# Performance work log

Measured on AMD Instinct MI355X. Metric: run time of the kernel, lower is better.

## Reference

```python
import jax, jax.numpy as jnp
import numpy as np

TOP_K = 8


def setup_inputs() -> dict:
    key = jax.random.key(0)
    k1, k2, k3 = jax.random.split(key, 3)
    tokens, hidden, experts = 32768, 2048, 64
    hidden_states = jax.random.normal(k1, (tokens, hidden), dtype=jnp.float32)
    weight = jax.random.normal(k2, (experts, hidden), dtype=jnp.float32) * 0.02
    bias = jax.random.normal(k3, (experts,), dtype=jnp.float32) * 0.02
    return {"hidden_states": hidden_states, "weight": weight, "bias": bias}


def reference(hidden_states, weight, bias):
    # router logits: [tokens, experts]
    logits = jnp.einsum('th,eh->te', hidden_states, weight) + bias
    top_vals, top_idx = jax.lax.top_k(logits, TOP_K)            # [tokens, k]
    top_probs = jax.nn.softmax(top_vals, axis=-1)               # softmax over selected k
    rows = jnp.arange(logits.shape[0])[:, None]                  # [tokens, 1]
    scores = jnp.zeros_like(logits).at[rows, top_idx].set(top_probs)
    return scores, top_idx
```

## Files before the change

kernel.cpp:

```cpp
#include <hip/hip_runtime.h>
#include <math.h>

typedef _Float16 half8 __attribute__((ext_vector_type(8)));
typedef _Float16 half4 __attribute__((ext_vector_type(4)));
typedef float    f32x4 __attribute__((ext_vector_type(4)));

#define TOKENS  32768
#define HIDDEN  2048
#define EXPERTS 64
#define TOPK    8
#define BKW     64
#define NWIN    (HIDDEN / BKW)
#define LDH     72

__global__ __launch_bounds__(256, 1)
void router_mfma(const float* __restrict__ A,
                 const float* __restrict__ W,
                 const float* __restrict__ bias,
                 float* __restrict__ out) {
    __shared__ __align__(16) _Float16 hsm[4 * 64 * LDH];
    _Float16* Ahs = hsm;
    _Float16* Als = hsm + 64 * LDH;
    _Float16* Whs = hsm + 2 * 64 * LDH;
    _Float16* Wls = hsm + 3 * 64 * LDH;

    const int tid = threadIdx.x;
    const int w   = tid >> 6;
    const int l   = tid & 63;
    const int g   = blockIdx.x;

    const int s_tok = tid >> 4;
    const int s_c   = tid & 15;
    const int we = tid >> 2;
    const int wc = tid & 3;

    const float* Abase = A + (size_t)g * 64 * HIDDEN;
    const float* WBase = W + (size_t)we * HIDDEN;

    f32x4 acc[4];
    #pragma unroll
    for (int n = 0; n < 4; ++n) acc[n] = (f32x4){0.f, 0.f, 0.f, 0.f};

    float4 ar0, ar1, ar2, ar3;
    float4 wr0, wr1, wr2, wr3;

    #define LOADA(win) do {                                                  \
        const float* p_ = Abase + (size_t)(win) * BKW + s_c * 4;             \
        ar0 = *(const float4*)(p_ + (size_t)(s_tok     ) * HIDDEN);          \
        ar1 = *(const float4*)(p_ + (size_t)(s_tok + 16) * HIDDEN);          \
        ar2 = *(const float4*)(p_ + (size_t)(s_tok + 32) * HIDDEN);          \
        ar3 = *(const float4*)(p_ + (size_t)(s_tok + 48) * HIDDEN);          \
    } while (0)

    #define LOADW(win) do {                                                  \
        const float* q_ = WBase + (size_t)(win) * BKW + wc * 8;              \
        wr0 = *(const float4*)(q_);                                          \
        wr1 = *(const float4*)(q_ + 4);                                      \
        wr2 = *(const float4*)(q_ + 32);                                     \
        wr3 = *(const float4*)(q_ + 36);                                     \
    } while (0)

    #define SPLIT4(HS, LS, v, OFF) do {                                      \
        _Float16 h0_ = (_Float16)(v).x, h1_ = (_Float16)(v).y;               \
        _Float16 h2_ = (_Float16)(v).z, h3_ = (_Float16)(v).w;               \
        half4 hh_ = {h0_, h1_, h2_, h3_};                                    \
        half4 ll_ = {(_Float16)((v).x - (float)h0_),                         \
                     (_Float16)((v).y - (float)h1_),                         \
                     (_Float16)((v).z - (float)h2_),                         \
                     (_Float16)((v).w - (float)h3_)};                        \
        *(half4*)(&(HS)[(OFF)]) = hh_;                                       \
        *(half4*)(&(LS)[(OFF)]) = ll_;                                       \
    } while (0)

    #define STAGE() do {                                                     \
        SPLIT4(Ahs, Als, ar0, (s_tok     ) * LDH + s_c * 4);                 \
        SPLIT4(Ahs, Als, ar1, (s_tok + 16) * LDH + s_c * 4);                 \
        SPLIT4(Ahs, Als, ar2, (s_tok + 32) * LDH + s_c * 4);                 \
        SPLIT4(Ahs, Als, ar3, (s_tok + 48) * LDH + s_c * 4);                 \
        SPLIT4(Whs, Wls, wr0, we * LDH + wc * 8);                            \
        SPLIT4(Whs, Wls, wr1, we * LDH + wc * 8 + 4);                        \
        SPLIT4(Whs, Wls, wr2, we * LDH + wc * 8 + 32);                       \
        SPLIT4(Whs, Wls, wr3, we * LDH + wc * 8 + 36);                       \
    } while (0)

    LOADA(0);
    LOADW(0);

    #pragma unroll 1
    for (int win = 0; win < NWIN; ++win) {
        __syncthreads();
        STAGE();
        __syncthreads();

        if (win + 1 < NWIN) {
            LOADA(win + 1);
            LOADW(win + 1);
        }

        #pragma unroll
        for (int ks = 0; ks < 2; ++ks) {
            const int ko = ks * 32 + (l >> 4) * 8;
            half8 ahi = *(const half8*)(&Ahs[(w * 16 + (l & 15)) * LDH + ko]);
            half8 alo = *(const half8*)(&Als[(w * 16 + (l & 15)) * LDH + ko]);
            #pragma unroll
            for (int n = 0; n < 4; ++n) {
                half8 bh = *(const half8*)(&Whs[(n * 16 + (l & 15)) * LDH + ko]);
                half8 bl = *(const half8*)(&Wls[(n * 16 + (l & 15)) * LDH + ko]);
                acc[n] = __builtin_amdgcn_mfma_f32_16x16x32_f16(ahi, bh, acc[n], 0, 0, 0);
                acc[n] = __builtin_amdgcn_mfma_f32_16x16x32_f16(ahi, bl, acc[n], 0, 0, 0);
                acc[n] = __builtin_amdgcn_mfma_f32_16x16x32_f16(alo, bh, acc[n], 0, 0, 0);
            }
        }
    }
    #undef LOADA
    #undef LOADW
    #undef SPLIT4
    #undef STAGE

    __syncthreads();
    float* lg = (float*)hsm;
    float* sc = (float*)hsm + 64 * 68;

    #pragma unroll
    for (int n = 0; n < 4; ++n) {
        float b = bias[n * 16 + (l & 15)];
        #pragma unroll
        for (int q = 0; q < 4; ++q) {
            int trow = w * 16 + (l >> 4) * 4 + q;
            lg[trow * 68 + n * 16 + (l & 15)] = acc[n][q] + b;
        }
    }
    for (int i = tid; i < 64 * 65; i += 256) sc[i] = 0.f;
    __syncthreads();

    if (tid < 64) {
        const int t = tid;
        float v[64];
        #pragma unroll
        for (int e = 0; e < 64; ++e) v[e] = lg[t * 68 + e];

        float tvals[TOPK]; int tix[TOPK]; float probs[TOPK];
        unsigned long long chosen = 0ull;
        #pragma unroll
        for (int j = 0; j < TOPK; ++j) {
            float best = -INFINITY; int bi = 0;
            #pragma unroll
            for (int e = 0; e < 64; ++e) {
                bool ok = ((chosen >> e) & 1ull) == 0ull;
                if (ok && v[e] > best) { best = v[e]; bi = e; }
            }
            chosen |= (1ull << bi);
            tvals[j] = best; tix[j] = bi;
        }
        float m = tvals[0];
        float ssum = 0.f;
        #pragma unroll
        for (int j = 0; j < TOPK; ++j) { probs[j] = __expf(tvals[j] - m); ssum += probs[j]; }
        float inv = 1.f / ssum;
        #pragma unroll
        for (int j = 0; j < TOPK; ++j) probs[j] *= inv;

        #pragma unroll
        for (int j = 0; j < TOPK; ++j) sc[t * 65 + tix[j]] = probs[j];

        float* oidx = out + (size_t)TOKENS * EXPERTS;
        const int token = g * 64 + t;
        #pragma unroll
        for (int j = 0; j < TOPK; ++j) oidx[(size_t)token * TOPK + j] = (float)tix[j];
    }
    __syncthreads();

    float* oscore = out + (size_t)g * 4096;
    #pragma unroll
    for (int p = 0; p < 4; ++p) {
        int fi  = tid + 256 * p;
        int tok = fi >> 4;
        int es  = (fi & 15) * 4;
        float4 vv;
        vv.x = sc[tok * 65 + es + 0];
        vv.y = sc[tok * 65 + es + 1];
        vv.z = sc[tok * 65 + es + 2];
        vv.w = sc[tok * 65 + es + 3];
        *(float4*)(oscore + (size_t)fi * 4) = vv;
    }
}

extern "C" void kernel_launch(void* const* d_in, const int* in_sizes, int n_in,
                              void* d_out, int out_size, void* d_ws, size_t ws_size,
                              hipStream_t stream) {
    const float* A    = (const float*)d_in[0];
    const float* W    = (const float*)d_in[1];
    const float* bias = (const float*)d_in[2];
    float* out = (float*)d_out;
    (void)d_ws; (void)ws_size;

    router_mfma<<<TOKENS / 64, 256, 0, stream>>>(A, W, bias, out);
}
```

Measured before the change: 61.21 us.

## Split K across two waves with 32-token blocks and LDS reduction

Cuts tokens per block from 64 to 32 and uses 128 threads (2 waves). Each wave takes half of every 64-wide K window and covers all 32 tokens, so the grid doubles to 1024 blocks. The two partial accumulators are summed through LDS before top-k. The aim is more blocks to fill the CUs and better hiding of HBM latency, at the cost of loading W once per 32 tokens instead of per 64 and an extra reduction step.

```diff
diff --git a/kernel.cpp b/kernel.cpp
--- a/kernel.cpp
+++ b/kernel.cpp
@@ -9,55 +9,58 @@
 #define HIDDEN  2048
 #define EXPERTS 64
 #define TOPK    8
+#define TB      32
 #define BKW     64
 #define NWIN    (HIDDEN / BKW)
 #define LDH     72
 
-__global__ __launch_bounds__(256, 1)
-void router_mfma(const float* __restrict__ A,
-                 const float* __restrict__ W,
-                 const float* __restrict__ bias,
-                 float* __restrict__ out) {
-    __shared__ __align__(16) _Float16 hsm[4 * 64 * LDH];
+__global__ __launch_bounds__(128, 1)
+void router_mfma32(const float* __restrict__ A,
+                   const float* __restrict__ W,
+                   const float* __restrict__ bias,
+                   float* __restrict__ out) {
+    __shared__ __align__(16) _Float16 hsm[(2 * TB + 2 * 64) * LDH];
     _Float16* Ahs = hsm;
-    _Float16* Als = hsm + 64 * LDH;
-    _Float16* Whs = hsm + 2 * 64 * LDH;
-    _Float16* Wls = hsm + 3 * 64 * LDH;
+    _Float16* Als = hsm + TB * LDH;
+    _Float16* Whs = hsm + 2 * TB * LDH;
+    _Float16* Wls = hsm + 2 * TB * LDH + 64 * LDH;
 
     const int tid = threadIdx.x;
-    const int w   = tid >> 6;
+    const int h   = tid >> 6;
     const int l   = tid & 63;
     const int g   = blockIdx.x;
 
-    const int s_tok = tid >> 4;
-    const int s_c   = tid & 15;
-    const int we = tid >> 2;
-    const int wc = tid & 3;
-
-    const float* Abase = A + (size_t)g * 64 * HIDDEN;
-    const float* WBase = W + (size_t)we * HIDDEN;
-
-    f32x4 acc[4];
+    const int a_r = tid >> 3;
+    const int a_c = tid & 7;
+    const int w_e = tid >> 1;
+    const int w_c = (tid & 1) * 8;
+
+    const float* Abase = A + (size_t)g * TB * HIDDEN;
+    const float* WBase = W + (size_t)w_e * HIDDEN;
+
+    f32x4 acc[2][4];
     #pragma unroll
-    for (int n = 0; n < 4; ++n) acc[n] = (f32x4){0.f, 0.f, 0.f, 0.f};
+    for (int s = 0; s < 2; ++s)
+        #pragma unroll
+        for (int n = 0; n < 4; ++n) acc[s][n] = (f32x4){0.f, 0.f, 0.f, 0.f};
 
     float4 ar0, ar1, ar2, ar3;
-    float4 wr0, wr1, wr2, wr3;
+    float4 wr0, wr1, wr2, wr3, wr4, wr5, wr6, wr7;
 
     #define LOADA(win) do {                                                  \
-        const float* p_ = Abase + (size_t)(win) * BKW + s_c * 4;             \
-        ar0 = *(const float4*)(p_ + (size_t)(s_tok     ) * HIDDEN);          \
-        ar1 = *(const float4*)(p_ + (size_t)(s_tok + 16) * HIDDEN);          \
-        ar2 = *(const float4*)(p_ + (size_t)(s_tok + 32) * HIDDEN);          \
-        ar3 = *(const float4*)(p_ + (size_t)(s_tok + 48) * HIDDEN);          \
+        const float* p_ = Abase + (size_t)(win) * BKW;                       \
+        ar0 = *(const float4*)(p_ + (size_t)(a_r     ) * HIDDEN + (a_c    ) * 4); \
+        ar1 = *(const float4*)(p_ + (size_t)(a_r     ) * HIDDEN + (a_c + 8) * 4); \
+        ar2 = *(const float4*)(p_ + (size_t)(a_r + 16) * HIDDEN + (a_c    ) * 4); \
+        ar3 = *(const float4*)(p_ + (size_t)(a_r + 16) * HIDDEN + (a_c + 8) * 4); \
     } while (0)
 
     #define LOADW(win) do {                                                  \
-        const float* q_ = WBase + (size_t)(win) * BKW + wc * 8;              \
-        wr0 = *(const float4*)(q_);                                          \
-        wr1 = *(const float4*)(q_ + 4);                                      \
-        wr2 = *(const float4*)(q_ + 32);                                     \
-        wr3 = *(const float4*)(q_ + 36);                                     \
+        const float* q_ = WBase + (size_t)(win) * BKW + w_c * 4;             \
+        wr0 = *(const float4*)(q_);      wr1 = *(const float4*)(q_ + 4);     \
+        wr2 = *(const float4*)(q_ + 8);  wr3 = *(const float4*)(q_ + 12);    \
+        wr4 = *(const float4*)(q_ + 16); wr5 = *(const float4*)(q_ + 20);    \
+        wr6 = *(const float4*)(q_ + 24); wr7 = *(const float4*)(q_ + 28);    \
     } while (0)
 
     #define SPLIT4(HS, LS, v, OFF) do {                                      \
@@ -73,18 +76,24 @@
     } while (0)
 
     #define STAGE() do {                                                     \
-        SPLIT4(Ahs, Als, ar0, (s_tok     ) * LDH + s_c * 4);                 \
-        SPLIT4(Ahs, Als, ar1, (s_tok + 16) * LDH + s_c * 4);                 \
-        SPLIT4(Ahs, Als, ar2, (s_tok + 32) * LDH + s_c * 4);                 \
-        SPLIT4(Ahs, Als, ar3, (s_tok + 48) * LDH + s_c * 4);                 \
-        SPLIT4(Whs, Wls, wr0, we * LDH + wc * 8);                            \
-        SPLIT4(Whs, Wls, wr1, we * LDH + wc * 8 + 4);                        \
-        SPLIT4(Whs, Wls, wr2, we * LDH + wc * 8 + 32);                       \
-        SPLIT4(Whs, Wls, wr3, we * LDH + wc * 8 + 36);                       \
+        SPLIT4(Ahs, Als, ar0, (a_r     ) * LDH + (a_c    ) * 4);             \
+        SPLIT4(Ahs, Als, ar1, (a_r     ) * LDH + (a_c + 8) * 4);             \
+        SPLIT4(Ahs, Als, ar2, (a_r + 16) * LDH + (a_c    ) * 4);             \
+        SPLIT4(Ahs, Als, ar3, (a_r + 16) * LDH + (a_c + 8) * 4);             \
+        SPLIT4(Whs, Wls, wr0, w_e * LDH + (w_c    ) * 4);                    \
+        SPLIT4(Whs, Wls, wr1, w_e * LDH + (w_c + 1) * 4);                    \
+        SPLIT4(Whs, Wls, wr2, w_e * LDH + (w_c + 2) * 4);                    \
+        SPLIT4(Whs, Wls, wr3, w_e * LDH + (w_c + 3) * 4);                    \
+        SPLIT4(Whs, Wls, wr4, w_e * LDH + (w_c + 4) * 4);                    \
+        SPLIT4(Whs, Wls, wr5, w_e * LDH + (w_c + 5) * 4);                    \
+        SPLIT4(Whs, Wls, wr6, w_e * LDH + (w_c + 6) * 4);                    \
+        SPLIT4(Whs, Wls, wr7, w_e * LDH + (w_c + 7) * 4);                    \
     } while (0)
 
     LOADA(0);
     LOADW(0);
+
+    const int ko = h * 32 + (l >> 4) * 8;
 
     #pragma unroll 1
     for (int win = 0; win < NWIN; ++win) {
@@ -98,17 +107,16 @@
         }
 
         #pragma unroll
-        for (int ks = 0; ks < 2; ++ks) {
-            const int ko = ks * 32 + (l >> 4) * 8;
-            half8 ahi = *(const half8*)(&Ahs[(w * 16 + (l & 15)) * LDH + ko]);
-            half8 alo = *(const half8*)(&Als[(w * 16 + (l & 15)) * LDH + ko]);
+        for (int s = 0; s < 2; ++s) {
+            half8 ahi = *(const half8*)(&Ahs[(s * 16 + (l & 15)) * LDH + ko]);
+            half8 alo = *(const half8*)(&Als[(s * 16 + (l & 15)) * LDH + ko]);
             #pragma unroll
             for (int n = 0; n < 4; ++n) {
                 half8 bh = *(const half8*)(&Whs[(n * 16 + (l & 15)) * LDH + ko]);
                 half8 bl = *(const half8*)(&Wls[(n * 16 + (l & 15)) * LDH + ko]);
-                acc[n] = __builtin_amdgcn_mfma_f32_16x16x32_f16(ahi, bh, acc[n], 0, 0, 0);
-                acc[n] = __builtin_amdgcn_mfma_f32_16x16x32_f16(ahi, bl, acc[n], 0, 0, 0);
-                acc[n] = __builtin_amdgcn_mfma_f32_16x16x32_f16(alo, bh, acc[n], 0, 0, 0);
+                acc[s][n] = __builtin_amdgcn_mfma_f32_16x16x32_f16(ahi, bh, acc[s][n], 0, 0, 0);
+                acc[s][n] = __builtin_amdgcn_mfma_f32_16x16x32_f16(ahi, bl, acc[s][n], 0, 0, 0);
+                acc[s][n] = __builtin_amdgcn_mfma_f32_16x16x32_f16(alo, bh, acc[s][n], 0, 0, 0);
             }
         }
     }
@@ -119,21 +127,35 @@
 
     __syncthreads();
     float* lg = (float*)hsm;
-    float* sc = (float*)hsm + 64 * 68;
-
-    #pragma unroll
-    for (int n = 0; n < 4; ++n) {
-        float b = bias[n * 16 + (l & 15)];
-        #pragma unroll
-        for (int q = 0; q < 4; ++q) {
-            int trow = w * 16 + (l >> 4) * 4 + q;
-            lg[trow * 68 + n * 16 + (l & 15)] = acc[n][q] + b;
-        }
-    }
-    for (int i = tid; i < 64 * 65; i += 256) sc[i] = 0.f;
-    __syncthreads();
-
-    if (tid < 64) {
+    float* sc = (float*)hsm + TB * 68;
+
+    if (h == 1) {
+        #pragma unroll
+        for (int s = 0; s < 2; ++s)
+            #pragma unroll
+            for (int n = 0; n < 4; ++n)
+                #pragma unroll
+                for (int q_ = 0; q_ < 4; ++q_)
+                    lg[(s * 16 + (l >> 4) * 4 + q_) * 68 + n * 16 + (l & 15)] = acc[s][n][q_];
+    }
+    __syncthreads();
+    if (h == 0) {
+        #pragma unroll
+        for (int s = 0; s < 2; ++s)
+            #pragma unroll
+            for (int n = 0; n < 4; ++n) {
+                float b = bias[n * 16 + (l & 15)];
+                #pragma unroll
+                for (int q_ = 0; q_ < 4; ++q_) {
+                    int idx = (s * 16 + (l >> 4) * 4 + q_) * 68 + n * 16 + (l & 15);
+                    lg[idx] = lg[idx] + acc[s][n][q_] + b;
+                }
+            }
+    }
+    for (int i = tid; i < TB * 65; i += 128) sc[i] = 0.f;
+    __syncthreads();
+
+    if (tid < TB) {
         const int t = tid;
         float v[64];
         #pragma unroll
@@ -164,16 +186,16 @@
         for (int j = 0; j < TOPK; ++j) sc[t * 65 + tix[j]] = probs[j];
 
         float* oidx = out + (size_t)TOKENS * EXPERTS;
-        const int token = g * 64 + t;
+        const int token = g * TB + t;
         #pragma unroll
         for (int j = 0; j < TOPK; ++j) oidx[(size_t)token * TOPK + j] = (float)tix[j];
     }
     __syncthreads();
 
-    float* oscore = out + (size_t)g * 4096;
+    float* oscore = out + (size_t)g * (TB * 64);
     #pragma unroll
     for (int p = 0; p < 4; ++p) {
-        int fi  = tid + 256 * p;
+        int fi  = tid + 128 * p;
         int tok = fi >> 4;
         int es  = (fi & 15) * 4;
         float4 vv;
@@ -194,5 +216,5 @@
     float* out = (float*)d_out;
     (void)d_ws; (void)ws_size;
 
-    router_mfma<<<TOKENS / 64, 256, 0, stream>>>(A, W, bias, out);
+    router_mfma32<<<TOKENS / TB, 128, 0, stream>>>(A, W, bias, out);
 }
```

After: 90.90 us. +48.5%, slower.

## Double-buffer LDS staging with two register sets and one barrier per window

Applied to the files above, without the earlier changes.

Splits shared memory into two fp16 hi/lo buffers and keeps two register sets of prefetched global data. MFMA compute on one buffer now overlaps with splitting and storing the next window into the other buffer, and prefetch runs two windows ahead. This removes one of the two barriers per window and the serial stage-then-compute ordering. In exchange, LDS use doubles, register pressure rises, and the custom barrier drops the final __syncthreads before the epilogue reuses shared memory.

```diff
diff --git a/kernel.cpp b/kernel.cpp
--- a/kernel.cpp
+++ b/kernel.cpp
@@ -12,18 +12,14 @@
 #define BKW     64
 #define NWIN    (HIDDEN / BKW)
 #define LDH     72
+#define BUFH    (4 * 64 * LDH)
 
 __global__ __launch_bounds__(256, 1)
-void router_mfma(const float* __restrict__ A,
-                 const float* __restrict__ W,
-                 const float* __restrict__ bias,
-                 float* __restrict__ out) {
-    __shared__ __align__(16) _Float16 hsm[4 * 64 * LDH];
-    _Float16* Ahs = hsm;
-    _Float16* Als = hsm + 64 * LDH;
-    _Float16* Whs = hsm + 2 * 64 * LDH;
-    _Float16* Wls = hsm + 3 * 64 * LDH;
-
+void router_rb(const float* __restrict__ A,
+               const float* __restrict__ W,
+               const float* __restrict__ bias,
+               float* __restrict__ out) {
+    __shared__ __align__(16) _Float16 hsm[2 * BUFH];
     const int tid = threadIdx.x;
     const int w   = tid >> 6;
     const int l   = tid & 63;
@@ -41,23 +37,23 @@
     #pragma unroll
     for (int n = 0; n < 4; ++n) acc[n] = (f32x4){0.f, 0.f, 0.f, 0.f};
 
-    float4 ar0, ar1, ar2, ar3;
-    float4 wr0, wr1, wr2, wr3;
-
-    #define LOADA(win) do {                                                  \
+    float4 arA0, arA1, arA2, arA3, wrA0, wrA1, wrA2, wrA3;
+    float4 arB0, arB1, arB2, arB3, wrB0, wrB1, wrB2, wrB3;
+
+    #define LOADA(S, win) do {                                               \
         const float* p_ = Abase + (size_t)(win) * BKW + s_c * 4;             \
-        ar0 = *(const float4*)(p_ + (size_t)(s_tok     ) * HIDDEN);          \
-        ar1 = *(const float4*)(p_ + (size_t)(s_tok + 16) * HIDDEN);          \
-        ar2 = *(const float4*)(p_ + (size_t)(s_tok + 32) * HIDDEN);          \
-        ar3 = *(const float4*)(p_ + (size_t)(s_tok + 48) * HIDDEN);          \
-    } while (0)
-
-    #define LOADW(win) do {                                                  \
+        ar##S##0 = *(const float4*)(p_ + (size_t)(s_tok     ) * HIDDEN);     \
+        ar##S##1 = *(const float4*)(p_ + (size_t)(s_tok + 16) * HIDDEN);     \
+        ar##S##2 = *(const float4*)(p_ + (size_t)(s_tok + 32) * HIDDEN);     \
+        ar##S##3 = *(const float4*)(p_ + (size_t)(s_tok + 48) * HIDDEN);     \
+    } while (0)
+
+    #define LOADW(S, win) do {                                               \
         const float* q_ = WBase + (size_t)(win) * BKW + wc * 8;              \
-        wr0 = *(const float4*)(q_);                                          \
-        wr1 = *(const float4*)(q_ + 4);                                      \
-        wr2 = *(const float4*)(q_ + 32);                                     \
-        wr3 = *(const float4*)(q_ + 36);                                     \
+        wr##S##0 = *(const float4*)(q_);                                     \
+        wr##S##1 = *(const float4*)(q_ + 4);                                 \
+        wr##S##2 = *(const float4*)(q_ + 32);                                \
+        wr##S##3 = *(const float4*)(q_ + 36);                                \
     } while (0)
 
     #define SPLIT4(HS, LS, v, OFF) do {                                      \
@@ -72,52 +68,73 @@
         *(half4*)(&(LS)[(OFF)]) = ll_;                                       \
     } while (0)
 
-    #define STAGE() do {                                                     \
-        SPLIT4(Ahs, Als, ar0, (s_tok     ) * LDH + s_c * 4);                 \
-        SPLIT4(Ahs, Als, ar1, (s_tok + 16) * LDH + s_c * 4);                 \
-        SPLIT4(Ahs, Als, ar2, (s_tok + 32) * LDH + s_c * 4);                 \
-        SPLIT4(Ahs, Als, ar3, (s_tok + 48) * LDH + s_c * 4);                 \
-        SPLIT4(Whs, Wls, wr0, we * LDH + wc * 8);                            \
-        SPLIT4(Whs, Wls, wr1, we * LDH + wc * 8 + 4);                        \
-        SPLIT4(Whs, Wls, wr2, we * LDH + wc * 8 + 32);                       \
-        SPLIT4(Whs, Wls, wr3, we * LDH + wc * 8 + 36);                       \
-    } while (0)
-
-    LOADA(0);
-    LOADW(0);
+    #define STAGE(S, B) do {                                                 \
+        _Float16* Ah_ = hsm + (B);                                           \
+        _Float16* Al_ = hsm + (B) + 64 * LDH;                                \
+        _Float16* Wh_ = hsm + (B) + 2 * 64 * LDH;                            \
+        _Float16* Wl_ = hsm + (B) + 3 * 64 * LDH;                            \
+        SPLIT4(Ah_, Al_, ar##S##0, (s_tok     ) * LDH + s_c * 4);            \
+        SPLIT4(Ah_, Al_, ar##S##1, (s_tok + 16) * LDH + s_c * 4);            \
+        SPLIT4(Ah_, Al_, ar##S##2, (s_tok + 32) * LDH + s_c * 4);            \
+        SPLIT4(Ah_, Al_, ar##S##3, (s_tok + 48) * LDH + s_c * 4);            \
+        SPLIT4(Wh_, Wl_, wr##S##0, we * LDH + wc * 8);                       \
+        SPLIT4(Wh_, Wl_, wr##S##1, we * LDH + wc * 8 + 4);                   \
+        SPLIT4(Wh_, Wl_, wr##S##2, we * LDH + wc * 8 + 32);                  \
+        SPLIT4(Wh_, Wl_, wr##S##3, we * LDH + wc * 8 + 36);                  \
+    } while (0)
+
+    #define COMPUTE(B) do {                                                  \
+        const _Float16* Ah_ = hsm + (B);                                     \
+        const _Float16* Al_ = hsm + (B) + 64 * LDH;                          \
+        const _Float16* Wh_ = hsm + (B) + 2 * 64 * LDH;                      \
+        const _Float16* Wl_ = hsm + (B) + 3 * 64 * LDH;                      \
+        _Pragma("unroll")                                                    \
+        for (int ks = 0; ks < 2; ++ks) {                                     \
+            const int ko = ks * 32 + (l >> 4) * 8;                           \
+            half8 ahi = *(const half8*)(&Ah_[(w * 16 + (l & 15)) * LDH + ko]); \
+            half8 alo = *(const half8*)(&Al_[(w * 16 + (l & 15)) * LDH + ko]); \
+            _Pragma("unroll")                                                \
+            for (int n = 0; n < 4; ++n) {                                    \
+                half8 bh = *(const half8*)(&Wh_[(n * 16 + (l & 15)) * LDH + ko]); \
+                half8 bl = *(const half8*)(&Wl_[(n * 16 + (l & 15)) * LDH + ko]); \
+                acc[n] = __builtin_amdgcn_mfma_f32_16x16x32_f16(ahi, bh, acc[n], 0, 0, 0); \
+                acc[n] = __builtin_amdgcn_mfma_f32_16x16x32_f16(ahi, bl, acc[n], 0, 0, 0); \
+                acc[n] = __builtin_amdgcn_mfma_f32_16x16x32_f16(alo, bh, acc[n], 0, 0, 0); \
+            }                                                                \
+        }                                                                    \
+    } while (0)
+
+    #define BAR() do {                                                       \
+        asm volatile("s_waitcnt lgkmcnt(0)" ::: "memory");                   \
+        __builtin_amdgcn_sched_barrier(0);                                   \
+        __builtin_amdgcn_s_barrier();                                        \
+        __builtin_amdgcn_sched_barrier(0);                                   \
+    } while (0)
+
+    LOADA(A, 0); LOADW(A, 0);
+    STAGE(A, 0);
+    LOADA(B, 1); LOADW(B, 1);
+    BAR();
 
     #pragma unroll 1
-    for (int win = 0; win < NWIN; ++win) {
-        __syncthreads();
-        STAGE();
-        __syncthreads();
-
-        if (win + 1 < NWIN) {
-            LOADA(win + 1);
-            LOADW(win + 1);
-        }
-
-        #pragma unroll
-        for (int ks = 0; ks < 2; ++ks) {
-            const int ko = ks * 32 + (l >> 4) * 8;
-            half8 ahi = *(const half8*)(&Ahs[(w * 16 + (l & 15)) * LDH + ko]);
-            half8 alo = *(const half8*)(&Als[(w * 16 + (l & 15)) * LDH + ko]);
-            #pragma unroll
-            for (int n = 0; n < 4; ++n) {
-                half8 bh = *(const half8*)(&Whs[(n * 16 + (l & 15)) * LDH + ko]);
-                half8 bl = *(const half8*)(&Wls[(n * 16 + (l & 15)) * LDH + ko]);
-                acc[n] = __builtin_amdgcn_mfma_f32_16x16x32_f16(ahi, bh, acc[n], 0, 0, 0);
-                acc[n] = __builtin_amdgcn_mfma_f32_16x16x32_f16(ahi, bl, acc[n], 0, 0, 0);
-                acc[n] = __builtin_amdgcn_mfma_f32_16x16x32_f16(alo, bh, acc[n], 0, 0, 0);
-            }
-        }
+    for (int s = 0; s < NWIN; s += 2) {
+        if (s + 2 < NWIN) { LOADA(A, s + 2); LOADW(A, s + 2); }
+        COMPUTE(0);
+        STAGE(B, BUFH);
+        BAR();
+
+        if (s + 3 < NWIN) { LOADA(B, s + 3); LOADW(B, s + 3); }
+        COMPUTE(BUFH);
+        if (s + 2 < NWIN) STAGE(A, 0);
+        BAR();
     }
     #undef LOADA
     #undef LOADW
     #undef SPLIT4
     #undef STAGE
-
-    __syncthreads();
+    #undef COMPUTE
+    #undef BAR
+
     float* lg = (float*)hsm;
     float* sc = (float*)hsm + 64 * 68;
 
@@ -194,5 +211,5 @@
     float* out = (float*)d_out;
     (void)d_ws; (void)ws_size;
 
-    router_mfma<<<TOKENS / 64, 256, 0, stream>>>(A, W, bias, out);
+    router_rb<<<TOKENS / 64, 256, 0, stream>>>(A, W, bias, out);
 }
```

Measured after the change: 67.25 us. +9.9%, slower.

## Halve block to two waves, each computing 32 token rows for B-fragment reuse

Applied to the files above, without the earlier changes.

Reduces the workgroup from 256 to 128 threads so each wave computes a 32x64 output tile with two accumulator sets, reusing each W fragment loaded from LDS across two A tiles. Global staging loads per thread double (8 A and 8 W float4s) to cover the same 64x64 window. This targets LDS read traffic and per-MFMA overhead, at the cost of fewer waves per block for hiding memory latency and higher register pressure.

```diff
diff --git a/kernel.cpp b/kernel.cpp
--- a/kernel.cpp
+++ b/kernel.cpp
@@ -13,11 +13,11 @@
 #define NWIN    (HIDDEN / BKW)
 #define LDH     72
 
-__global__ __launch_bounds__(256, 1)
-void router_mfma(const float* __restrict__ A,
-                 const float* __restrict__ W,
-                 const float* __restrict__ bias,
-                 float* __restrict__ out) {
+__global__ __launch_bounds__(128, 1)
+void router_w2(const float* __restrict__ A,
+               const float* __restrict__ W,
+               const float* __restrict__ bias,
+               float* __restrict__ out) {
     __shared__ __align__(16) _Float16 hsm[4 * 64 * LDH];
     _Float16* Ahs = hsm;
     _Float16* Als = hsm + 64 * LDH;
@@ -31,33 +31,39 @@
 
     const int s_tok = tid >> 4;
     const int s_c   = tid & 15;
-    const int we = tid >> 2;
-    const int wc = tid & 3;
+    const int we = tid >> 1;
+    const int wc = tid & 1;
 
     const float* Abase = A + (size_t)g * 64 * HIDDEN;
     const float* WBase = W + (size_t)we * HIDDEN;
 
-    f32x4 acc[4];
+    f32x4 acc[2][4];
     #pragma unroll
-    for (int n = 0; n < 4; ++n) acc[n] = (f32x4){0.f, 0.f, 0.f, 0.f};
-
-    float4 ar0, ar1, ar2, ar3;
-    float4 wr0, wr1, wr2, wr3;
+    for (int s = 0; s < 2; ++s)
+        #pragma unroll
+        for (int n = 0; n < 4; ++n) acc[s][n] = (f32x4){0.f, 0.f, 0.f, 0.f};
+
+    float4 ar0, ar1, ar2, ar3, ar4, ar5, ar6, ar7;
+    float4 wr0, wr1, wr2, wr3, wr4, wr5, wr6, wr7;
 
     #define LOADA(win) do {                                                  \
         const float* p_ = Abase + (size_t)(win) * BKW + s_c * 4;             \
         ar0 = *(const float4*)(p_ + (size_t)(s_tok     ) * HIDDEN);          \
-        ar1 = *(const float4*)(p_ + (size_t)(s_tok + 16) * HIDDEN);          \
-        ar2 = *(const float4*)(p_ + (size_t)(s_tok + 32) * HIDDEN);          \
-        ar3 = *(const float4*)(p_ + (size_t)(s_tok + 48) * HIDDEN);          \
+        ar1 = *(const float4*)(p_ + (size_t)(s_tok +  8) * HIDDEN);          \
+        ar2 = *(const float4*)(p_ + (size_t)(s_tok + 16) * HIDDEN);          \
+        ar3 = *(const float4*)(p_ + (size_t)(s_tok + 24) * HIDDEN);          \
+        ar4 = *(const float4*)(p_ + (size_t)(s_tok + 32) * HIDDEN);          \
+        ar5 = *(const float4*)(p_ + (size_t)(s_tok + 40) * HIDDEN);          \
+        ar6 = *(const float4*)(p_ + (size_t)(s_tok + 48) * HIDDEN);          \
+        ar7 = *(const float4*)(p_ + (size_t)(s_tok + 56) * HIDDEN);          \
     } while (0)
 
     #define LOADW(win) do {                                                  \
-        const float* q_ = WBase + (size_t)(win) * BKW + wc * 8;              \
-        wr0 = *(const float4*)(q_);                                          \
-        wr1 = *(const float4*)(q_ + 4);                                      \
-        wr2 = *(const float4*)(q_ + 32);                                     \
-        wr3 = *(const float4*)(q_ + 36);                                     \
+        const float* q_ = WBase + (size_t)(win) * BKW + wc * 32;             \
+        wr0 = *(const float4*)(q_);       wr1 = *(const float4*)(q_ + 4);    \
+        wr2 = *(const float4*)(q_ + 8);   wr3 = *(const float4*)(q_ + 12);   \
+        wr4 = *(const float4*)(q_ + 16);  wr5 = *(const float4*)(q_ + 20);   \
+        wr6 = *(const float4*)(q_ + 24);  wr7 = *(const float4*)(q_ + 28);   \
     } while (0)
 
     #define SPLIT4(HS, LS, v, OFF) do {                                      \
@@ -74,13 +80,21 @@
 
     #define STAGE() do {                                                     \
         SPLIT4(Ahs, Als, ar0, (s_tok     ) * LDH + s_c * 4);                 \
-        SPLIT4(Ahs, Als, ar1, (s_tok + 16) * LDH + s_c * 4);                 \
-        SPLIT4(Ahs, Als, ar2, (s_tok + 32) * LDH + s_c * 4);                 \
-        SPLIT4(Ahs, Als, ar3, (s_tok + 48) * LDH + s_c * 4);                 \
-        SPLIT4(Whs, Wls, wr0, we * LDH + wc * 8);                            \
-        SPLIT4(Whs, Wls, wr1, we * LDH + wc * 8 + 4);                        \
-        SPLIT4(Whs, Wls, wr2, we * LDH + wc * 8 + 32);                       \
-        SPLIT4(Whs, Wls, wr3, we * LDH + wc * 8 + 36);                       \
+        SPLIT4(Ahs, Als, ar1, (s_tok +  8) * LDH + s_c * 4);                 \
+        SPLIT4(Ahs, Als, ar2, (s_tok + 16) * LDH + s_c * 4);                 \
+        SPLIT4(Ahs, Als, ar3, (s_tok + 24) * LDH + s_c * 4);                 \
+        SPLIT4(Ahs, Als, ar4, (s_tok + 32) * LDH + s_c * 4);                 \
+        SPLIT4(Ahs, Als, ar5, (s_tok + 40) * LDH + s_c * 4);                 \
+        SPLIT4(Ahs, Als, ar6, (s_tok + 48) * LDH + s_c * 4);                 \
+        SPLIT4(Ahs, Als, ar7, (s_tok + 56) * LDH + s_c * 4);                 \
+        SPLIT4(Whs, Wls, wr0, we * LDH + wc * 32);                           \
+        SPLIT4(Whs, Wls, wr1, we * LDH + wc * 32 + 4);                       \
+        SPLIT4(Whs, Wls, wr2, we * LDH + wc * 32 + 8);                       \
+        SPLIT4(Whs, Wls, wr3, we * LDH + wc * 32 + 12);                      \
+        SPLIT4(Whs, Wls, wr4, we * LDH + wc * 32 + 16);                      \
+        SPLIT4(Whs, Wls, wr5, we * LDH + wc * 32 + 20);                      \
+        SPLIT4(Whs, Wls, wr6, we * LDH + wc * 32 + 24);                      \
+        SPLIT4(Whs, Wls, wr7, we * LDH + wc * 32 + 28);                      \
     } while (0)
 
     LOADA(0);
@@ -100,15 +114,20 @@
         #pragma unroll
         for (int ks = 0; ks < 2; ++ks) {
             const int ko = ks * 32 + (l >> 4) * 8;
-            half8 ahi = *(const half8*)(&Ahs[(w * 16 + (l & 15)) * LDH + ko]);
-            half8 alo = *(const half8*)(&Als[(w * 16 + (l & 15)) * LDH + ko]);
+            half8 ahi0 = *(const half8*)(&Ahs[(w * 32 +      (l & 15)) * LDH + ko]);
+            half8 alo0 = *(const half8*)(&Als[(w * 32 +      (l & 15)) * LDH + ko]);
+            half8 ahi1 = *(const half8*)(&Ahs[(w * 32 + 16 + (l & 15)) * LDH + ko]);
+            half8 alo1 = *(const half8*)(&Als[(w * 32 + 16 + (l & 15)) * LDH + ko]);
             #pragma unroll
             for (int n = 0; n < 4; ++n) {
                 half8 bh = *(const half8*)(&Whs[(n * 16 + (l & 15)) * LDH + ko]);
                 half8 bl = *(const half8*)(&Wls[(n * 16 + (l & 15)) * LDH + ko]);
-                acc[n] = __builtin_amdgcn_mfma_f32_16x16x32_f16(ahi, bh, acc[n], 0, 0, 0);
-                acc[n] = __builtin_amdgcn_mfma_f32_16x16x32_f16(ahi, bl, acc[n], 0, 0, 0);
-                acc[n] = __builtin_amdgcn_mfma_f32_16x16x32_f16(alo, bh, acc[n], 0, 0, 0);
+                acc[0][n] = __builtin_amdgcn_mfma_f32_16x16x32_f16(ahi0, bh, acc[0][n], 0, 0, 0);
+                acc[0][n] = __builtin_amdgcn_mfma_f32_16x16x32_f16(ahi0, bl, acc[0][n], 0, 0, 0);
+                acc[0][n] = __builtin_amdgcn_mfma_f32_16x16x32_f16(alo0, bh, acc[0][n], 0, 0, 0);
+                acc[1][n] = __builtin_amdgcn_mfma_f32_16x16x32_f16(ahi1, bh, acc[1][n], 0, 0, 0);
+                acc[1][n] = __builtin_amdgcn_mfma_f32_16x16x32_f16(ahi1, bl, acc[1][n], 0, 0, 0);
+                acc[1][n] = __builtin_amdgcn_mfma_f32_16x16x32_f16(alo1, bh, acc[1][n], 0, 0, 0);
             }
         }
     }
@@ -122,15 +141,17 @@
     float* sc = (float*)hsm + 64 * 68;
 
     #pragma unroll
-    for (int n = 0; n < 4; ++n) {
-        float b = bias[n * 16 + (l & 15)];
-        #pragma unroll
-        for (int q = 0; q < 4; ++q) {
-            int trow = w * 16 + (l >> 4) * 4 + q;
-            lg[trow * 68 + n * 16 + (l & 15)] = acc[n][q] + b;
-        }
-    }
-    for (int i = tid; i < 64 * 65; i += 256) sc[i] = 0.f;
+    for (int s = 0; s < 2; ++s)
+        #pragma unroll
+        for (int n = 0; n < 4; ++n) {
+            float b = bias[n * 16 + (l & 15)];
+            #pragma unroll
+            for (int q = 0; q < 4; ++q) {
+                int trow = w * 32 + s * 16 + (l >> 4) * 4 + q;
+                lg[trow * 68 + n * 16 + (l & 15)] = acc[s][n][q] + b;
+            }
+        }
+    for (int i = tid; i < 64 * 65; i += 128) sc[i] = 0.f;
     __syncthreads();
 
     if (tid < 64) {
@@ -172,8 +193,8 @@
 
     float* oscore = out + (size_t)g * 4096;
     #pragma unroll
-    for (int p = 0; p < 4; ++p) {
-        int fi  = tid + 256 * p;
+    for (int p = 0; p < 8; ++p) {
+        int fi  = tid + 128 * p;
         int tok = fi >> 4;
         int es  = (fi & 15) * 4;
         float4 vv;
@@ -194,5 +215,5 @@
     float* out = (float*)d_out;
     (void)d_ws; (void)ws_size;
 
-    router_mfma<<<TOKENS / 64, 256, 0, stream>>>(A, W, bias, out);
+    router_w2<<<TOKENS / 64, 128, 0, stream>>>(A, W, bias, out);
 }
```

Measured after the change: 81.63 us. +33.3%, slower.
